# Kernel optimization log

Hardware: AMD Instinct MI355X
Metric: run time of the kernel (lower is better)

## Reference

```python
import jax, jax.numpy as jnp
import numpy as np

INPUT_SIZE = 1024
ATTN_SIZE = 1024


def setup_inputs() -> dict:
    key = jax.random.key(0)
    ks = jax.random.split(key, 7)
    s = 1.0 / np.sqrt(INPUT_SIZE)
    x = jax.random.normal(ks[0], (2048, 8, INPUT_SIZE), dtype=jnp.float32)
    Wq = jax.random.uniform(ks[1], (ATTN_SIZE, INPUT_SIZE), jnp.float32, -s, s)
    bq = jax.random.uniform(ks[2], (ATTN_SIZE,), jnp.float32, -s, s)
    Wk = jax.random.uniform(ks[3], (ATTN_SIZE, INPUT_SIZE), jnp.float32, -s, s)
    bk = jax.random.uniform(ks[4], (ATTN_SIZE,), jnp.float32, -s, s)
    Wv = jax.random.uniform(ks[5], (ATTN_SIZE, INPUT_SIZE), jnp.float32, -s, s)
    bv = jax.random.uniform(ks[6], (ATTN_SIZE,), jnp.float32, -s, s)
    return {"x": x, "Wq": Wq, "bq": bq, "Wk": Wk, "bk": bk, "Wv": Wv, "bv": bv}


def reference(x, Wq, bq, Wk, bk, Wv, bv):
    # x: (S, B, D) -> (B, S, D)
    xb = jnp.swapaxes(x, 0, 1)
    Q = jnp.einsum('bsd,ad->bsa', xb, Wq) + bq  # (B, S, A)
    K = jnp.einsum('bsd,ad->bsa', xb, Wk) + bk
    V = jnp.einsum('bsd,ad->bsa', xb, Wv) + bv
    S = Q.shape[1]
    scores = jnp.einsum('bqa,bka->bqk', Q, K) / jnp.sqrt(jnp.float32(ATTN_SIZE))
    causal = jnp.tril(jnp.ones((S, S), dtype=bool))  # True where attended
    scores = jnp.where(causal, scores, -jnp.inf)
    probs = jax.nn.softmax(scores, axis=-1)
    out = jnp.einsum('bqk,bka->bqa', probs, V)  # (B, S, A)
    return jnp.swapaxes(out, 0, 1)  # (S, B, A)
```

## Files before the change

### kernel.cpp

```cpp
#include <hip/hip_runtime.h>
#include <hip/hip_bf16.h>
#include <math.h>

typedef short bf16x8 __attribute__((ext_vector_type(8)));
typedef float f32x4 __attribute__((ext_vector_type(4)));
typedef short short4v __attribute__((ext_vector_type(4)));
typedef short short8v __attribute__((ext_vector_type(8)));

__device__ __forceinline__ short f2bf(float f) {
  unsigned u = __builtin_bit_cast(unsigned, f);
  unsigned r = (u + 0x7FFFu + ((u >> 16) & 1u)) >> 16;
  return (short)r;
}
__device__ __forceinline__ float bf2f(short s) {
  unsigned u = ((unsigned)(unsigned short)s) << 16;
  return __builtin_bit_cast(float, u);
}

typedef __attribute__((address_space(1))) const unsigned g_u32;
typedef __attribute__((address_space(3))) unsigned l_u32;
__device__ __forceinline__ void gload_lds16(const short* g, short* l) {
  __builtin_amdgcn_global_load_lds((g_u32*)g, (l_u32*)l, 16, 0, 0);
}

#define VMCNT(n) asm volatile("s_waitcnt vmcnt(" #n ")" ::: "memory")


__global__ __launch_bounds__(256) void k_cast_x(const float* __restrict__ x, short* __restrict__ xb) {
  int tid = blockIdx.x * 256 + threadIdx.x;
  int d4 = tid & 255;
  int sb = tid >> 8;
  int s = sb & 2047;
  int b = sb >> 11;
  float4 v = *((const float4*)(x + (((size_t)s * 8 + b) << 10)) + d4);
  short4v o;
  o.x = f2bf(v.x); o.y = f2bf(v.y); o.z = f2bf(v.z); o.w = f2bf(v.w);
  *((short4v*)(xb + (((size_t)b * 2048 + s) << 10)) + d4) = o;
}

__global__ __launch_bounds__(256) void k_cast_w(const float* __restrict__ Wq, const float* __restrict__ Wk,
                                                const float* __restrict__ Wv, short* __restrict__ Wcat) {
  int tid = blockIdx.x * 256 + threadIdx.x;
  int d4 = tid & 255;
  int n = tid >> 8;
  const float* src = (n < 1024) ? Wq : (n < 2048 ? Wk : Wv);
  int nl = n & 1023;
  float4 v = *((const float4*)(src + ((size_t)nl << 10)) + d4);
  short4v o;
  o.x = f2bf(v.x); o.y = f2bf(v.y); o.z = f2bf(v.z); o.w = f2bf(v.w);
  *((short4v*)(Wcat + ((size_t)n << 10)) + d4) = o;
}

__global__ __launch_bounds__(256) void k_cast_bias(const float* __restrict__ bq, const float* __restrict__ bk,
                                                   const float* __restrict__ bv, float* __restrict__ biascat) {
  int i = blockIdx.x * 256 + threadIdx.x;
  if (i < 3072) biascat[i] = (i < 1024) ? bq[i] : (i < 2048 ? bk[i & 1023] : bv[i & 1023]);
}

template <int LDA, int LDB>
__device__ __forceinline__ void gemm128n_core(const short* __restrict__ Ag, const short* __restrict__ Bg,
                                              int NC, short* __restrict__ lds, f32x4 (&acc)[4][4], int tid) {
  const int lane = tid & 63;
  const int wid = tid >> 6;
  const int wm = wid >> 1, wn = wid & 1;
  const int r15 = lane & 15;
  const int g = lane >> 4;
  const int co = ((g ^ ((r15 >> 1) & 3)) << 3);
  short* As = lds;
  short* Bs = lds + 3 * 8192;

  const int abase = (wm * 64 + r15) * 32 + co;
  const int bbase = (wn * 64 + r15) * 32 + co;

  auto stage_pair = [&](int c) {
    short* Ap = As + (c % 3) * 8192;
    short* Bp = Bs + (c % 3) * 4096;
    int kb = c << 5;
#pragma unroll
    for (int i = 0; i < 2; ++i) {
      int ch = i * 512 + tid;
      int r = ch >> 2, s = ch & 3;
      gload_lds16(Ag + (size_t)r * LDA + kb + ((s ^ ((r >> 1) & 3)) << 3), Ap + ch * 8);
    }
    {
      int r = tid >> 2, s = tid & 3;
      gload_lds16(Bg + (size_t)r * LDB + kb + ((s ^ ((r >> 1) & 3)) << 3), Bp + tid * 8);
    }
  };

  auto phase = [&](int c, bool stage, bool last) {
    bf16x8 a4[4], br[4];
    const short* pa = As + (c % 3) * 8192 + abase;
    const short* pb = Bs + (c % 3) * 4096 + bbase;
#pragma unroll
    for (int mf = 0; mf < 4; ++mf) a4[mf] = *(const bf16x8*)(pa + mf * 512);
#pragma unroll
    for (int nf = 0; nf < 4; ++nf) br[nf] = *(const bf16x8*)(pb + nf * 512);
    if (stage) {
      stage_pair(c + 2);
      VMCNT(3);
    } else if (!last) {
      VMCNT(0);
    }
    __builtin_amdgcn_s_barrier();
    asm volatile("s_waitcnt lgkmcnt(0)" ::: "memory");
    __builtin_amdgcn_sched_barrier(0);
    __builtin_amdgcn_s_setprio(1);
#pragma unroll
    for (int mf = 0; mf < 4; ++mf)
#pragma unroll
      for (int nf = 0; nf < 4; ++nf)
        acc[mf][nf] = __builtin_amdgcn_mfma_f32_16x16x32_bf16(a4[mf], br[nf], acc[mf][nf], 0, 0, 0);
    __builtin_amdgcn_s_setprio(0);
    __builtin_amdgcn_s_barrier();
  };

  stage_pair(0);
  stage_pair(1);
  VMCNT(3);
  __builtin_amdgcn_s_barrier();

  for (int c = 0; c < NC - 2; ++c) phase(c, true, false);
  phase(NC - 2, false, false);
  phase(NC - 1, false, true);
}

__global__ __launch_bounds__(512, 4) void k_proj(const short* __restrict__ Xb, const short* __restrict__ Wc,
                                                 const float* __restrict__ biascat,
                                                 short* __restrict__ Q, short* __restrict__ K, short* __restrict__ Vt) {
  __shared__ __align__(16) short lds[36864];
  int tid = threadIdx.x;
  int wg = blockIdx.x;
  int swz = (wg & 7) * 192 + (wg >> 3);
  int mt = swz / 24, nt = swz % 24;
  int m0 = mt << 8, n0 = nt << 7;
  f32x4 acc[4][4] = {};
  gemm128n_core<1024, 1024>(Xb + (size_t)m0 * 1024, Wc + (size_t)n0 * 1024, 32, lds, acc, tid);
  int lane = tid & 63, wid = tid >> 6;
  int wm = wid >> 1, wn = wid & 1;
  int r15 = lane & 15, g = lane >> 4;
  int which = n0 >> 10;
  int nbase = n0 & 1023;
  if (which == 2) {
#pragma unroll
    for (int ni = 0; ni < 4; ++ni) {
      int cth = wn * 64 + ni * 16 + r15;
      int a = nbase + cth;
      float bv = biascat[n0 + cth];
#pragma unroll
      for (int mi = 0; mi < 4; ++mi) {
        int r = m0 + wm * 64 + mi * 16 + g * 4;
        int b = r >> 11, s = r & 2047;
        short4v o;
#pragma unroll
        for (int j = 0; j < 4; ++j) o[j] = f2bf(acc[mi][ni][j] + bv);
        *(short4v*)(Vt + ((size_t)b << 21) + ((size_t)a << 11) + s) = o;
      }
    }
  } else {
    short* outb = (which == 0) ? Q : K;
#pragma unroll
    for (int ni = 0; ni < 4; ++ni) {
      int cth = wn * 64 + ni * 16 + r15;
      float bv = biascat[n0 + cth];
#pragma unroll
      for (int mi = 0; mi < 4; ++mi)
#pragma unroll
        for (int j = 0; j < 4; ++j) {
          int r = m0 + wm * 64 + mi * 16 + g * 4 + j;
          outb[((size_t)r << 10) + nbase + cth] = f2bf(acc[mi][ni][j] + bv);
        }
    }
  }
}

__global__ __launch_bounds__(512, 4) void k_qk(const short* __restrict__ Q, const short* __restrict__ K,
                                               short* __restrict__ Sc) {
  __shared__ __align__(16) short lds[36864];
  int f = blockIdx.x;
  int b = f & 7;
  int idx = f >> 3;
  int mt = (int)((sqrtf(4.f * idx + 1.f) - 1.f) * 0.5f);
  while ((mt + 1) * (mt + 2) <= idx) ++mt;
  while (mt * (mt + 1) > idx) --mt;
  int nt = idx - mt * (mt + 1);
  int tid = threadIdx.x;
  int m0 = mt << 8, n0 = nt << 7;
  const short* Qb = Q + ((size_t)b << 21);
  const short* Kb = K + ((size_t)b << 21);
  f32x4 acc[4][4] = {};
  gemm128n_core<1024, 1024>(Qb + (size_t)m0 * 1024, Kb + (size_t)n0 * 1024, 32, lds, acc, tid);
  short* Sb = Sc + ((size_t)b << 22);
  int lane = tid & 63, wid = tid >> 6;
  int wm = wid >> 1, wn = wid & 1;
  int r15 = lane & 15, g = lane >> 4;
#pragma unroll
  for (int mi = 0; mi < 4; ++mi)
#pragma unroll
    for (int ni = 0; ni < 4; ++ni)
#pragma unroll
      for (int j = 0; j < 4; ++j) {
        int r = m0 + wm * 64 + mi * 16 + g * 4 + j;
        int c = n0 + wn * 64 + ni * 16 + r15;
        Sb[((size_t)r << 11) + c] = f2bf(acc[mi][ni][j] * 0.03125f);
      }
}

__global__ __launch_bounds__(256) void k_softmax(short* __restrict__ Sc) {
  int row = blockIdx.x;
  int b = row >> 11, q = row & 2047;
  short* Pr = Sc + ((size_t)b << 22) + ((size_t)q << 11);
  int T = ((q >> 8) + 1) << 8;
  int tid = threadIdx.x, lane = tid & 63, wid = tid >> 6;
  int k0 = tid << 3;
  float v[8];
  if (k0 < T) {
    short8v raw = *(const short8v*)(Pr + k0);
#pragma unroll
    for (int j = 0; j < 8; ++j) v[j] = (k0 + j <= q) ? bf2f(raw[j]) : -__builtin_inff();
  } else {
#pragma unroll
    for (int j = 0; j < 8; ++j) v[j] = -__builtin_inff();
  }
  float mx = v[0];
#pragma unroll
  for (int j = 1; j < 8; ++j) mx = fmaxf(mx, v[j]);
  for (int off = 1; off < 64; off <<= 1) mx = fmaxf(mx, __shfl_xor(mx, off, 64));
  __shared__ float red[2][4];
  if (lane == 0) red[0][wid] = mx;
  __syncthreads();
  mx = fmaxf(fmaxf(red[0][0], red[0][1]), fmaxf(red[0][2], red[0][3]));
  float e[8], sum = 0.f;
#pragma unroll
  for (int j = 0; j < 8; ++j) {
    e[j] = exp2f((v[j] - mx) * 1.4426950408889634f);
    sum += e[j];
  }
  for (int off = 1; off < 64; off <<= 1) sum += __shfl_xor(sum, off, 64);
  if (lane == 0) red[1][wid] = sum;
  __syncthreads();
  sum = red[1][0] + red[1][1] + red[1][2] + red[1][3];
  float inv = 1.f / sum;
  if (k0 < T) {
    short8v o;
#pragma unroll
    for (int j = 0; j < 8; ++j) o[j] = (k0 + j <= q) ? f2bf(e[j] * inv) : (short)0;
    *(short8v*)(Pr + k0) = o;
  }
}

__global__ __launch_bounds__(512, 4) void k_pv(const short* __restrict__ P, const short* __restrict__ Vt,
                                               float* __restrict__ out) {
  __shared__ __align__(16) short lds[36864];
  int f = blockIdx.x;
  int b = f & 7;
  int idx = f >> 3;
  int half = idx >> 5, j = idx & 31;
  int mt = half ? (7 - (j >> 2)) : (j >> 2);
  int nt = half ? (4 + (j & 3)) : (j & 3);
  int tid = threadIdx.x;
  int m0 = mt << 8, n0 = nt << 7;
  int NC = 8 * (mt + 1);
  const short* Pb = P + ((size_t)b << 22);
  const short* Vtb = Vt + ((size_t)b << 21);
  f32x4 acc[4][4] = {};
  gemm128n_core<2048, 2048>(Pb + (size_t)m0 * 2048, Vtb + (size_t)n0 * 2048, NC, lds, acc, tid);
  int lane = tid & 63, wid = tid >> 6;
  int wm = wid >> 1, wn = wid & 1;
  int r15 = lane & 15, g = lane >> 4;
#pragma unroll
  for (int mi = 0; mi < 4; ++mi)
#pragma unroll
    for (int ni = 0; ni < 4; ++ni)
#pragma unroll
      for (int j2 = 0; j2 < 4; ++j2) {
        int r = m0 + wm * 64 + mi * 16 + g * 4 + j2;
        int c = n0 + wn * 64 + ni * 16 + r15;
        out[((size_t)r << 13) + ((size_t)b << 10) + c] = acc[mi][ni][j2];
      }
}

extern "C" void kernel_launch(void* const* d_in, const int* in_sizes, int n_in,
                              void* d_out, int out_size, void* d_ws, size_t ws_size,
                              hipStream_t stream) {
  const float* x  = (const float*)d_in[0];
  const float* Wq = (const float*)d_in[1];
  const float* bq = (const float*)d_in[2];
  const float* Wk = (const float*)d_in[3];
  const float* bk = (const float*)d_in[4];
  const float* Wv = (const float*)d_in[5];
  const float* bv = (const float*)d_in[6];
  float* out = (float*)d_out;
  char* ws = (char*)d_ws;

  short* xb   = (short*)(ws);
  short* Wcat = (short*)(ws + 33554432);
  float* bias = (float*)(ws + 39845888);
  short* Q    = (short*)(ws + 39858176);
  short* K    = (short*)(ws + 73412608);
  short* Vt   = (short*)(ws + 106967040);
  short* Sc   = (short*)(ws + 140521472);

  k_cast_x<<<16384, 256, 0, stream>>>(x, xb);
  k_cast_w<<<3072, 256, 0, stream>>>(Wq, Wk, Wv, Wcat);
  k_cast_bias<<<12, 256, 0, stream>>>(bq, bk, bv, bias);
  k_proj<<<1536, 512, 0, stream>>>(xb, Wcat, bias, Q, K, Vt);
  k_qk<<<576, 512, 0, stream>>>(Q, K, Sc);
  k_softmax<<<16384, 256, 0, stream>>>(Sc);
  k_pv<<<512, 512, 0, stream>>>(Sc, Vt, out);
}
```

Baseline: 259.3 us.

## Use 256x256 projection tiles and one-wave-per-row softmax

The QKV projection GEMM moves from 256x128 tiles to 256x256 tiles, using a new double-buffered core with K-step 64, 8 waves arranged 2x4, and a 128 KB LDS footprint, with occupancy lowered to one block per CU. This raises arithmetic intensity and halves the B-operand reloads per output. Softmax now uses one wavefront per row instead of one 256-thread block, which drops the LDS reductions and __syncthreads. The cost is lower occupancy and more barriers in the GEMM, which makes latency hiding harder.

Measured after the change: 256.2 us. Within noise of the previous version (-1.2%).

```diff
diff --git a/kernel.cpp b/kernel.cpp
--- a/kernel.cpp
+++ b/kernel.cpp
@@ -58,6 +58,90 @@
 }
 
 template <int LDA, int LDB>
+__device__ __forceinline__ void gemm256h_core(const short* __restrict__ Ag, const short* __restrict__ Bg,
+                                              int NT, short* __restrict__ lds, f32x4 (&acc)[8][4], int tid) {
+  const int lane = tid & 63;
+  const int wid = tid >> 6;
+  const int wm = wid >> 2, wn = wid & 3;
+  const int r15 = lane & 15;
+  const int g = lane >> 4;
+  const int co = ((g ^ ((r15 >> 1) & 3)) << 3);
+  short* As = lds;
+  short* Bs = lds + 32768;
+
+  auto stageA = [&](int t, int kk) {
+    short* Lp = As + (((t & 1) * 2 + kk) << 13);
+    int kb = (t << 6) + (kk << 5);
+#pragma unroll
+    for (int i = 0; i < 2; ++i) {
+      int ch = i * 512 + tid;
+      int r = ch >> 2, s = ch & 3;
+      gload_lds16(Ag + (size_t)r * LDA + kb + ((s ^ ((r >> 1) & 3)) << 3), Lp + ch * 8);
+    }
+  };
+  auto stageB = [&](int t, int kk) {
+    short* Lp = Bs + (((t & 1) * 2 + kk) << 13);
+    int kb = (t << 6) + (kk << 5);
+#pragma unroll
+    for (int i = 0; i < 2; ++i) {
+      int ch = i * 512 + tid;
+      int r = ch >> 2, s = ch & 3;
+      gload_lds16(Bg + (size_t)r * LDB + kb + ((s ^ ((r >> 1) & 3)) << 3), Lp + ch * 8);
+    }
+  };
+
+  bf16x8 a4[4], br[4];
+  auto rdA = [&](int t, int kk, int mh) {
+    const short* p = As + (((t & 1) * 2 + kk) << 13) + (wm * 128 + mh * 64 + r15) * 32 + co;
+#pragma unroll
+    for (int mf = 0; mf < 4; ++mf) a4[mf] = *(const bf16x8*)(p + mf * 512);
+  };
+  auto rdB = [&](int t, int kk) {
+    const short* p = Bs + (((t & 1) * 2 + kk) << 13) + (wn * 64 + r15) * 32 + co;
+#pragma unroll
+    for (int nf = 0; nf < 4; ++nf) br[nf] = *(const bf16x8*)(p + nf * 512);
+  };
+  auto mm = [&](int mh) {
+    __builtin_amdgcn_s_setprio(1);
+#pragma unroll
+    for (int mf = 0; mf < 4; ++mf)
+#pragma unroll
+      for (int nf = 0; nf < 4; ++nf)
+        acc[mh * 4 + mf][nf] =
+            __builtin_amdgcn_mfma_f32_16x16x32_bf16(a4[mf], br[nf], acc[mh * 4 + mf][nf], 0, 0, 0);
+    __builtin_amdgcn_s_setprio(0);
+  };
+
+  stageA(0, 0); stageB(0, 0); stageA(0, 1); stageB(0, 1);
+  VMCNT(4);
+  __builtin_amdgcn_s_barrier();
+
+  for (int t = 0; t < NT; ++t) {
+    const bool more = (t + 1 < NT);
+    rdA(t, 0, 0); rdB(t, 0);
+    if (more) stageA(t + 1, 0);
+    __builtin_amdgcn_s_barrier();
+    mm(0);
+    __builtin_amdgcn_s_barrier();
+    rdA(t, 0, 1);
+    if (more) { stageB(t + 1, 0); VMCNT(4); } else { VMCNT(0); }
+    __builtin_amdgcn_s_barrier();
+    mm(1);
+    __builtin_amdgcn_s_barrier();
+    rdA(t, 1, 0); rdB(t, 1);
+    if (more) stageA(t + 1, 1);
+    __builtin_amdgcn_s_barrier();
+    mm(0);
+    __builtin_amdgcn_s_barrier();
+    rdA(t, 1, 1);
+    if (more) { stageB(t + 1, 1); VMCNT(4); }
+    __builtin_amdgcn_s_barrier();
+    mm(1);
+    __builtin_amdgcn_s_barrier();
+  }
+}
+
+template <int LDA, int LDB>
 __device__ __forceinline__ void gemm128n_core(const short* __restrict__ Ag, const short* __restrict__ Bg,
                                               int NC, short* __restrict__ lds, f32x4 (&acc)[4][4], int tid) {
   const int lane = tid & 63;
@@ -125,19 +209,19 @@
   phase(NC - 1, false, true);
 }
 
-__global__ __launch_bounds__(512, 4) void k_proj(const short* __restrict__ Xb, const short* __restrict__ Wc,
+__global__ __launch_bounds__(512, 1) void k_proj(const short* __restrict__ Xb, const short* __restrict__ Wc,
                                                  const float* __restrict__ biascat,
                                                  short* __restrict__ Q, short* __restrict__ K, short* __restrict__ Vt) {
-  __shared__ __align__(16) short lds[36864];
+  __shared__ __align__(16) short lds[65536];
   int tid = threadIdx.x;
   int wg = blockIdx.x;
-  int swz = (wg & 7) * 192 + (wg >> 3);
-  int mt = swz / 24, nt = swz % 24;
-  int m0 = mt << 8, n0 = nt << 7;
-  f32x4 acc[4][4] = {};
-  gemm128n_core<1024, 1024>(Xb + (size_t)m0 * 1024, Wc + (size_t)n0 * 1024, 32, lds, acc, tid);
+  int swz = (wg & 7) * 96 + (wg >> 3);
+  int mt = swz / 12, nt = swz % 12;
+  int m0 = mt << 8, n0 = nt << 8;
+  f32x4 acc[8][4] = {};
+  gemm256h_core<1024, 1024>(Xb + (size_t)m0 * 1024, Wc + (size_t)n0 * 1024, 16, lds, acc, tid);
   int lane = tid & 63, wid = tid >> 6;
-  int wm = wid >> 1, wn = wid & 1;
+  int wm = wid >> 2, wn = wid & 3;
   int r15 = lane & 15, g = lane >> 4;
   int which = n0 >> 10;
   int nbase = n0 & 1023;
@@ -148,8 +232,8 @@
       int a = nbase + cth;
       float bv = biascat[n0 + cth];
 #pragma unroll
-      for (int mi = 0; mi < 4; ++mi) {
-        int r = m0 + wm * 64 + mi * 16 + g * 4;
+      for (int mi = 0; mi < 8; ++mi) {
+        int r = m0 + wm * 128 + (mi >> 2) * 64 + (mi & 3) * 16 + g * 4;
         int b = r >> 11, s = r & 2047;
         short4v o;
 #pragma unroll
@@ -164,10 +248,10 @@
       int cth = wn * 64 + ni * 16 + r15;
       float bv = biascat[n0 + cth];
 #pragma unroll
-      for (int mi = 0; mi < 4; ++mi)
+      for (int mi = 0; mi < 8; ++mi)
 #pragma unroll
         for (int j = 0; j < 4; ++j) {
-          int r = m0 + wm * 64 + mi * 16 + g * 4 + j;
+          int r = m0 + wm * 128 + (mi >> 2) * 64 + (mi & 3) * 16 + g * 4 + j;
           outb[((size_t)r << 10) + nbase + cth] = f2bf(acc[mi][ni][j] + bv);
         }
     }
@@ -207,45 +291,51 @@
 }
 
 __global__ __launch_bounds__(256) void k_softmax(short* __restrict__ Sc) {
-  int row = blockIdx.x;
+  int row = blockIdx.x * 4 + (threadIdx.x >> 6);
+  int lane = threadIdx.x & 63;
   int b = row >> 11, q = row & 2047;
   short* Pr = Sc + ((size_t)b << 22) + ((size_t)q << 11);
   int T = ((q >> 8) + 1) << 8;
-  int tid = threadIdx.x, lane = tid & 63, wid = tid >> 6;
-  int k0 = tid << 3;
-  float v[8];
-  if (k0 < T) {
-    short8v raw = *(const short8v*)(Pr + k0);
-#pragma unroll
-    for (int j = 0; j < 8; ++j) v[j] = (k0 + j <= q) ? bf2f(raw[j]) : -__builtin_inff();
-  } else {
-#pragma unroll
-    for (int j = 0; j < 8; ++j) v[j] = -__builtin_inff();
+  float v[4][8];
+  float mx = -__builtin_inff();
+#pragma unroll
+  for (int it = 0; it < 4; ++it) {
+    int k0 = it * 512 + lane * 8;
+    if (k0 < T) {
+      short8v raw = *(const short8v*)(Pr + k0);
+#pragma unroll
+      for (int j = 0; j < 8; ++j) {
+        float x = (k0 + j <= q) ? bf2f(raw[j]) : -__builtin_inff();
+        v[it][j] = x;
+        mx = fmaxf(mx, x);
+      }
+    }
   }
-  float mx = v[0];
-#pragma unroll
-  for (int j = 1; j < 8; ++j) mx = fmaxf(mx, v[j]);
   for (int off = 1; off < 64; off <<= 1) mx = fmaxf(mx, __shfl_xor(mx, off, 64));
-  __shared__ float red[2][4];
-  if (lane == 0) red[0][wid] = mx;
-  __syncthreads();
-  mx = fmaxf(fmaxf(red[0][0], red[0][1]), fmaxf(red[0][2], red[0][3]));
-  float e[8], sum = 0.f;
-#pragma unroll
-  for (int j = 0; j < 8; ++j) {
-    e[j] = exp2f((v[j] - mx) * 1.4426950408889634f);
-    sum += e[j];
+  float sum = 0.f;
+#pragma unroll
+  for (int it = 0; it < 4; ++it) {
+    int k0 = it * 512 + lane * 8;
+    if (k0 < T) {
+#pragma unroll
+      for (int j = 0; j < 8; ++j) {
+        float e = exp2f((v[it][j] - mx) * 1.4426950408889634f);
+        v[it][j] = e;
+        sum += e;
+      }
+    }
   }
   for (int off = 1; off < 64; off <<= 1) sum += __shfl_xor(sum, off, 64);
-  if (lane == 0) red[1][wid] = sum;
-  __syncthreads();
-  sum = red[1][0] + red[1][1] + red[1][2] + red[1][3];
   float inv = 1.f / sum;
-  if (k0 < T) {
-    short8v o;
-#pragma unroll
-    for (int j = 0; j < 8; ++j) o[j] = (k0 + j <= q) ? f2bf(e[j] * inv) : (short)0;
-    *(short8v*)(Pr + k0) = o;
+#pragma unroll
+  for (int it = 0; it < 4; ++it) {
+    int k0 = it * 512 + lane * 8;
+    if (k0 < T) {
+      short8v o;
+#pragma unroll
+      for (int j = 0; j < 8; ++j) o[j] = (k0 + j <= q) ? f2bf(v[it][j] * inv) : (short)0;
+      *(short8v*)(Pr + k0) = o;
+    }
   }
 }
 
@@ -304,8 +394,8 @@
   k_cast_x<<<16384, 256, 0, stream>>>(x, xb);
   k_cast_w<<<3072, 256, 0, stream>>>(Wq, Wk, Wv, Wcat);
   k_cast_bias<<<12, 256, 0, stream>>>(bq, bk, bv, bias);
-  k_proj<<<1536, 512, 0, stream>>>(xb, Wcat, bias, Q, K, Vt);
+  k_proj<<<768, 512, 0, stream>>>(xb, Wcat, bias, Q, K, Vt);
   k_qk<<<576, 512, 0, stream>>>(Q, K, Sc);
-  k_softmax<<<16384, 256, 0, stream>>>(Sc);
+  k_softmax<<<4096, 256, 0, stream>>>(Sc);
   k_pv<<<512, 512, 0, stream>>>(Sc, Vt, out);
 }
```
